# Kernel tuning notes

Hardware: AMD Instinct MI355X
Metric: run time of the kernel (lower is better)

Reference implementation:

```python
import jax, jax.numpy as jnp
import numpy as np

B, S, E, H = 2, 2048, 1024, 16
D = E // H          # head_dim = 64
HK = H // 4         # heads per kernel group = 4
MASKED_BIAS = -10000.0


def _dwconv_causal(x, w, b):
    # x: [B, h, S, D], w: [D, k], b: [D]; causal depthwise conv along S
    k = w.shape[1]
    s = x.shape[2]
    xp = jnp.pad(x, ((0, 0), (0, 0), (k - 1, 0), (0, 0)))
    out = b
    for i in range(k):
        out = out + xp[:, :, i:i + s, :] * w[:, i]
    return out


def setup_inputs() -> dict:
    key = jax.random.key(0)
    ks = jax.random.split(key, 32)
    inp = {
        'hidden_states': jax.random.normal(ks[0], (B, S, E), jnp.float32),
        'c_attn_w': jax.random.normal(ks[1], (E, 3 * E), jnp.float32) * 0.02,
        'c_attn_b': jnp.zeros((3 * E,), jnp.float32),
        'c_proj_w': jax.random.normal(ks[2], (E, E), jnp.float32) * 0.02,
        'c_proj_b': jnp.zeros((E,), jnp.float32),
    }
    i = 3
    for pre in ('q', 'k', 'v'):
        for kern in (3, 5, 7):
            inp[f'{pre}w{kern}'] = jax.random.normal(ks[i], (D, kern), jnp.float32) * (1.0 / kern)
            inp[f'{pre}b{kern}'] = jnp.zeros((D,), jnp.float32)
            i += 1
    return inp


def _forward(hidden_states, c_attn_w, c_attn_b, c_proj_w, c_proj_b,
             qw3, qb3, qw5, qb5, qw7, qb7,
             kw3, kb3, kw5, kb5, kw7, kb7,
             vw3, vb3, vw5, vb5, vw7, vb7):
    qkv = hidden_states @ c_attn_w + c_attn_b            # [B,S,3E]
    q, k, v = jnp.split(qkv, 3, axis=-1)

    def split_heads(t):
        return t.reshape(B, S, H, D).transpose(0, 2, 1, 3)  # [B,H,S,D]

    q, k, v = split_heads(q), split_heads(k), split_heads(v)

    def tranception_mix(t, ws_bs):
        parts = [t[:, :HK]]
        for g, (w, b) in enumerate(ws_bs):
            parts.append(_dwconv_causal(t[:, (g + 1) * HK:(g + 2) * HK], w, b))
        return jnp.concatenate(parts, axis=1)

    q = tranception_mix(q, [(qw3, qb3), (qw5, qb5), (qw7, qb7)])
    k = tranception_mix(k, [(kw3, kb3), (kw5, kb5), (kw7, kb7)])
    v = tranception_mix(v, [(vw3, vb3), (vw5, vb5), (vw7, vb7)])

    scores = jnp.einsum('bhqd,bhkd->bhqk', q, k) / jnp.sqrt(jnp.float32(D))
    causal = jnp.tril(jnp.ones((S, S), bool))
    scores = jnp.where(causal, scores, jnp.float32(MASKED_BIAS))
    attn = jax.nn.softmax(scores, axis=-1)
    out = jnp.einsum('bhqk,bhkd->bhqd', attn, v)
    out = out.transpose(0, 2, 1, 3).reshape(B, S, E)
    return out @ c_proj_w + c_proj_b


def reference(hidden_states, c_attn_w, c_attn_b, c_proj_w, c_proj_b,
              qw3, qb3, qw5, qb5, qw7, qb7,
              kw3, kb3, kw5, kb5, kw7, kb7,
              vw3, vb3, vw5, vb5, vw7, vb7):
    return _forward(hidden_states, c_attn_w, c_attn_b, c_proj_w, c_proj_b,
                    qw3, qb3, qw5, qb5, qw7, qb7,
                    kw3, kb3, kw5, kb5, kw7, kb7,
                    vw3, vb3, vw5, vb5, vw7, vb7)
```

## Files before the change

kernel.cpp:

```cpp
#include <hip/hip_runtime.h>
#include <stdint.h>
#include <math.h>

typedef unsigned short u16;
typedef __attribute__((ext_vector_type(8))) short short8;
typedef __attribute__((ext_vector_type(4))) float floatx4;

#define DEV static __device__ __forceinline__

struct alignas(8) us4 { u16 x, y, z, w; };
struct alignas(16) us8 { u16 v[8]; };
struct alignas(16) f4 { float x, y, z, w; };
struct alignas(8) f2 { float x, y; };
struct alignas(8) u32x2 { uint32_t x, y; };

DEV u16 f2bf(float f) {
  uint32_t u = __float_as_uint(f);
  u += 0x7fffu + ((u >> 16) & 1u);
  return (u16)(u >> 16);
}
DEV float bf2f(u16 h) { return __uint_as_float(((uint32_t)h) << 16); }

DEV uint32_t pkbf(float a, float b) {
#if __has_builtin(__builtin_amdgcn_cvt_pk_bf16_f32)
  typedef __attribute__((ext_vector_type(2))) __bf16 bf2_t;
  bf2_t v = __builtin_amdgcn_cvt_pk_bf16_f32(a, b);
  uint32_t r; __builtin_memcpy(&r, &v, 4); return r;
#else
  return (uint32_t)f2bf(a) | ((uint32_t)f2bf(b) << 16);
#endif
}

DEV float fexp2(float x) {
#if __has_builtin(__builtin_amdgcn_exp2f)
  return __builtin_amdgcn_exp2f(x);
#else
  return exp2f(x);
#endif
}

DEV void load_lds16(const void* g, void* l) {
  __builtin_amdgcn_global_load_lds((const __attribute__((address_space(1))) void*)g,
                                   (__attribute__((address_space(3))) void*)l, 16, 0, 0);
}

__global__ __launch_bounds__(256) void prep_fused(const float* __restrict__ hidden, u16* __restrict__ h_bf,
                                                  const float* __restrict__ attn_w, u16* __restrict__ wqkvT,
                                                  const float* __restrict__ proj_w, u16* __restrict__ wprojT) {
  __shared__ float tile[32][33];
  const int bx = blockIdx.x;
  const int t = threadIdx.x;
  if (bx < 4096) {
    const int i = (bx * 256 + t) * 4;
    f4 v = *(const f4*)(hidden + i);
    us4 o; o.x = f2bf(v.x); o.y = f2bf(v.y); o.z = f2bf(v.z); o.w = f2bf(v.w);
    *(us4*)(h_bf + i) = o;
    return;
  }
  const float* in; u16* out; int K, N, n0, k0;
  if (bx < 7168) {
    const int bid = bx - 4096;
    in = attn_w; out = wqkvT; K = 1024; N = 3072;
    n0 = (bid % 96) * 32; k0 = (bid / 96) * 32;
  } else {
    const int bid = bx - 7168;
    in = proj_w; out = wprojT; K = 1024; N = 1024;
    n0 = (bid & 31) * 32; k0 = (bid >> 5) * 32;
  }
  const int tx = t & 31, ty = t >> 5;
  for (int i = ty; i < 32; i += 8)
    tile[i][tx] = in[(size_t)(k0 + i) * N + n0 + tx];
  __syncthreads();
  for (int i = ty; i < 32; i += 8)
    out[(size_t)(n0 + i) * K + k0 + tx] = f2bf(tile[tx][i]);
}

template <int EPI, int BN, int NGRP>
__global__ __launch_bounds__(256) void gemm_bt(const u16* __restrict__ A,
                                               const u16* __restrict__ Bt,
                                               const float* __restrict__ bias,
                                               void* __restrict__ outp,
                                               int M, int N, int K) {
  constexpr int NT = BN / 32;
  __shared__ u16 lA[128 * 64];
  __shared__ u16 lB[BN * 64];
  const int t = threadIdx.x;
  const int w = t >> 6, lane = t & 63;
  const int quad = lane >> 4, l15 = lane & 15;
  const int wm = w >> 1, wn = w & 1;
  const int wn_off = wn * (BN / 2);

  const int bid = blockIdx.x;
  const int gsz = 32 * NGRP;
  const int grp = bid / gsz;
  const int r = bid - grp * gsz;
  const int m0 = (r & 31) * 128;
  const int n0 = (grp * NGRP + (r >> 5)) * BN;

  floatx4 acc[4][NT] = {};

  const int srow = t >> 3;
  const int scol = (((t & 7) ^ (srow & 7)) << 3);
  const u16* gA = A + (size_t)(m0 + srow) * K + scol;
  const u16* gB = Bt + (size_t)(n0 + srow) * K + scol;
  u16* sA = lA + t * 8;
  u16* sB = lB + t * 8;
  const size_t rstep = (size_t)32 * K;

  for (int k0 = 0; k0 < K; k0 += 64) {
#pragma unroll
    for (int c = 0; c < 4; c++) load_lds16(gA + c * rstep, sA + c * 2048);
#pragma unroll
    for (int c = 0; c < BN / 32; c++) load_lds16(gB + c * rstep, sB + c * 2048);
    gA += 64; gB += 64;
    __syncthreads();
#pragma unroll
    for (int kc = 0; kc < 2; kc++) {
      short8 af[4], bfr[NT];
#pragma unroll
      for (int mt = 0; mt < 4; mt++)
        af[mt] = *(const short8*)&lA[(wm * 64 + mt * 16 + l15) * 64 + (((kc * 4 + quad) ^ (l15 & 7)) << 3)];
#pragma unroll
      for (int nt = 0; nt < NT; nt++)
        bfr[nt] = *(const short8*)&lB[(wn_off + nt * 16 + l15) * 64 + (((kc * 4 + quad) ^ (l15 & 7)) << 3)];
#pragma unroll
      for (int mt = 0; mt < 4; mt++)
#pragma unroll
        for (int nt = 0; nt < NT; nt++)
          acc[mt][nt] = __builtin_amdgcn_mfma_f32_16x16x32_bf16(bfr[nt], af[mt], acc[mt][nt], 0, 0, 0);
    }
    __syncthreads();
  }

  if (EPI == 0) {
    u16* outq = (u16*)outp;
#pragma unroll
    for (int nt = 0; nt < NT; nt++) {
      const int nb = n0 + wn_off + nt * 16 + quad * 4;
      const f4 bn4 = *(const f4*)&bias[nb];
      const int tensor = nb >> 10, e = nb & 1023;
      const int h = e >> 6, d = e & 63;
      const size_t abase = (size_t)tensor * 4194304 + (size_t)h * 131072 + d;
#pragma unroll
      for (int mt = 0; mt < 4; mt++) {
        const int rr = m0 + wm * 64 + mt * 16 + l15;
        const int b = rr >> 11, s = rr & 2047;
        u32x2 o;
        o.x = pkbf(acc[mt][nt][0] + bn4.x, acc[mt][nt][1] + bn4.y);
        o.y = pkbf(acc[mt][nt][2] + bn4.z, acc[mt][nt][3] + bn4.w);
        *(u32x2*)&outq[abase + (size_t)b * 2097152 + (size_t)s * 64] = o;
      }
    }
  } else {
    float* outf = (float*)outp;
#pragma unroll
    for (int nt = 0; nt < NT; nt++) {
      const int nb = n0 + wn_off + nt * 16 + quad * 4;
      const f4 bn4 = *(const f4*)&bias[nb];
#pragma unroll
      for (int mt = 0; mt < 4; mt++) {
        const int rr = m0 + wm * 64 + mt * 16 + l15;
        f4 o;
        o.x = acc[mt][nt][0] + bn4.x;
        o.y = acc[mt][nt][1] + bn4.y;
        o.z = acc[mt][nt][2] + bn4.z;
        o.w = acc[mt][nt][3] + bn4.w;
        *(f4*)&outf[(size_t)rr * N + nb] = o;
      }
    }
  }
}

struct ConvW { const float* w[9]; const float* b[9]; };

template <int K>
DEV void conv_run(const u16* xt, int sl0, int d, const float* wp, const float* bp,
                  float qscale, float* out32) {
  float wr[K];
#pragma unroll
  for (int j = 0; j < K; j++) wr[j] = wp[d * K + j];
  const float br = bp[d];
  float win[K];
#pragma unroll
  for (int m = 1; m < K; m++) win[m] = bf2f(xt[(sl0 + 6 - K + m) * 68 + d]);
#pragma unroll
  for (int i = 0; i < 32; i++) {
#pragma unroll
    for (int m = 0; m < K - 1; m++) win[m] = win[m + 1];
    win[K - 1] = bf2f(xt[(sl0 + 6 + i) * 68 + d]);
    float val = br;
#pragma unroll
    for (int j = 0; j < K; j++) val += wr[j] * win[j];
    out32[i] = val * qscale;
  }
}

__global__ __launch_bounds__(256) void conv_mix(const u16* __restrict__ qkv, ConvW cw,
                                                u16* __restrict__ qpost,
                                                u16* __restrict__ kpost,
                                                u16* __restrict__ vpostT) {
  __shared__ u16 xt[134 * 68];
  __shared__ u16 yt[64 * 136];
  const int t = threadIdx.x;
  const int s0 = blockIdx.x * 128;
  const int h = blockIdx.y;
  const int tz = blockIdx.z;
  const int tensor = tz >> 1, b = tz & 1;
  const u16* src = qkv + (((size_t)tensor * 2 + b) * 16 + h) * 131072;

  for (int idx = t; idx < 134 * 16; idx += 256) {
    const int row = idx >> 4, c4 = (idx & 15) << 2;
    const int s = s0 - 6 + row;
    us4 v = {0, 0, 0, 0};
    if (s >= 0) v = *(const us4*)&src[(size_t)s * 64 + c4];
    *(us4*)&xt[row * 68 + c4] = v;
  }
  __syncthreads();

  const int group = h >> 2;
  const float* wp = (group > 0) ? cw.w[tensor * 3 + group - 1] : nullptr;
  const float* bp = (group > 0) ? cw.b[tensor * 3 + group - 1] : nullptr;
  const float qscale = (tensor == 0) ? 0.18033688f : 1.0f;

  const int d = t & 63;
  const int sl0 = (t >> 6) * 32;

  float out32[32];
  if (group == 0) {
#pragma unroll
    for (int i = 0; i < 32; i++)
      out32[i] = bf2f(xt[(sl0 + 6 + i) * 68 + d]) * qscale;
  } else if (group == 1) {
    conv_run<3>(xt, sl0, d, wp, bp, qscale, out32);
  } else if (group == 2) {
    conv_run<5>(xt, sl0, d, wp, bp, qscale, out32);
  } else {
    conv_run<7>(xt, sl0, d, wp, bp, qscale, out32);
  }

  if (tensor < 2) {
    u16* outp = (tensor == 0) ? qpost : kpost;
    const size_t ob = (((size_t)b * 16 + h) * 2048 + s0) * 64;
#pragma unroll
    for (int i = 0; i < 32; i++)
      outp[ob + (size_t)(sl0 + i) * 64 + d] = f2bf(out32[i]);
  } else {
#pragma unroll
    for (int i = 0; i < 32; i++)
      yt[d * 136 + sl0 + i] = f2bf(out32[i]);
    __syncthreads();
    const size_t ob = ((size_t)b * 16 + h) * 64;
    const int sl = (t & 15) * 8;
#pragma unroll
    for (int pass = 0; pass < 4; pass++) {
      const int dd = (t >> 4) + pass * 16;
      us8 vv = *(const us8*)&yt[dd * 136 + sl];
      *(us8*)&vpostT[(ob + dd) * 2048 + s0 + sl] = vv;
    }
  }
}

__global__ __launch_bounds__(256) void attn_fwd(const u16* __restrict__ Q,
                                                const u16* __restrict__ Kp,
                                                const u16* __restrict__ Vt,
                                                u16* __restrict__ Out,
                                                u16* __restrict__ Opart,
                                                f2* __restrict__ ml) {
  __shared__ u16 lK[2][128 * 64];
  __shared__ u16 lV[2][64 * 128];
  __shared__ u16 lP[4][32 * 64];
  const int t = threadIdx.x;
  const int w = t >> 6, lane = t & 63;
  const int quad = lane >> 4, l15 = lane & 15;
  const int e7 = l15 & 7;

  const int lin = blockIdx.x;
  const int xcd = lin & 7;
  const int idx = lin >> 3;
  const int grp = idx / 72;
  const int u = idx - grp * 72;
  const int bh = grp * 8 + xcd;
  int p = (int)(0.5f * (sqrtf(4.0f * (float)u + 1.0f) - 1.0f));
  if ((p + 1) * (p + 2) <= u) p++;
  if (p * (p + 1) > u) p--;
  const int v = u - p * (p + 1);
  const int qi = 2 * p + (v >= p + 1 ? 1 : 0);
  const int slab = v - (v >= p + 1 ? p + 1 : 0);
  const int ns = (qi + 2) >> 1;
  const int jbeg = slab * 2;
  const int nh = min(2, qi + 1 - jbeg);

  const int b = bh >> 4, h = bh & 15;
  const size_t qkbase = (size_t)bh * 131072;
  const int qblk = qi * 128 + w * 32;

  const int krow = t >> 3;
  const int kcol = (((t & 7) ^ (krow & 7)) << 3);
  const u16* gK = Kp + qkbase + (size_t)krow * 64 + kcol;
  const int vrow = t >> 4;
  const int vcol = (((t & 15) ^ vrow) << 3);
  const u16* gV = Vt + qkbase + (size_t)vrow * 2048 + vcol;
  u16* myP = lP[w];

  {
    const int j0 = jbeg * 128;
    u16* sK = &lK[0][0] + t * 8;
    u16* sV = &lV[0][0] + t * 8;
#pragma unroll
    for (int c = 0; c < 4; c++) {
      load_lds16(gK + (size_t)(j0 + c * 32) * 64, sK + c * 2048);
      load_lds16(gV + j0 + c * 16 * 2048, sV + c * 2048);
    }
  }
  asm volatile("" ::: "memory");

  short8 qf[2][2];
#pragma unroll
  for (int qt = 0; qt < 2; qt++)
#pragma unroll
    for (int kc = 0; kc < 2; kc++)
      qf[qt][kc] = *(const short8*)&Q[qkbase + (size_t)(qblk + qt * 16 + l15) * 64 + kc * 32 + quad * 8];
  asm volatile("" ::: "memory");

  if (nh == 2) {
    const int j0 = (jbeg + 1) * 128;
    u16* sK = &lK[1][0] + t * 8;
    u16* sV = &lV[1][0] + t * 8;
#pragma unroll
    for (int c = 0; c < 4; c++) {
      load_lds16(gK + (size_t)(j0 + c * 32) * 64, sK + c * 2048);
      load_lds16(gV + j0 + c * 16 * 2048, sV + c * 2048);
    }
    asm volatile("s_waitcnt vmcnt(12)" ::: "memory");
  } else {
    asm volatile("s_waitcnt vmcnt(4)" ::: "memory");
  }
  __builtin_amdgcn_s_barrier();

  float lst[2] = {0.0f, 0.0f};
  floatx4 accO[4][2] = {};

  for (int hf = 0; hf < nh; hf++) {
    if (hf == 1) {
      asm volatile("s_waitcnt vmcnt(0)" ::: "memory");
      __builtin_amdgcn_s_barrier();
    }
    const int j = jbeg + hf;
    const int j0 = j * 128;
    const u16* cK = lK[hf];
    const u16* cV = lV[hf];

    floatx4 accS[8][2] = {};
    __builtin_amdgcn_s_setprio(1);
#pragma unroll
    for (int kvt = 0; kvt < 8; kvt++) {
#pragma unroll
      for (int kc = 0; kc < 2; kc++) {
        const short8 a = *(const short8*)&cK[(kvt * 16 + l15) * 64 + (((kc * 4 + quad) ^ e7) << 3)];
#pragma unroll
        for (int qt = 0; qt < 2; qt++)
          accS[kvt][qt] = __builtin_amdgcn_mfma_f32_16x16x32_bf16(a, qf[qt][kc], accS[kvt][qt], 0, 0, 0);
      }
    }
    __builtin_amdgcn_s_setprio(0);

    if (j == qi) {
#pragma unroll
      for (int qt = 0; qt < 2; qt++) {
        const int q = qblk + qt * 16 + l15;
#pragma unroll
        for (int kvt = 0; kvt < 8; kvt++)
#pragma unroll
          for (int r = 0; r < 4; r++) {
            const int kv = j0 + kvt * 16 + quad * 4 + r;
            if (kv > q) accS[kvt][qt][r] = -3.0e38f;
          }
      }
    }

    uint32_t pk01[2][8], pk23[2][8];
#pragma unroll
    for (int qt = 0; qt < 2; qt++) {
      float ts = 0.0f;
#pragma unroll
      for (int kvt = 0; kvt < 8; kvt++) {
        const float p0 = fexp2(accS[kvt][qt][0]);
        const float p1 = fexp2(accS[kvt][qt][1]);
        const float p2 = fexp2(accS[kvt][qt][2]);
        const float p3 = fexp2(accS[kvt][qt][3]);
        ts += (p0 + p1) + (p2 + p3);
        pk01[qt][kvt] = pkbf(p0, p1);
        pk23[qt][kvt] = pkbf(p2, p3);
      }
      lst[qt] += ts;
    }

#pragma unroll
    for (int kvh = 0; kvh < 2; kvh++) {
#pragma unroll
      for (int qt = 0; qt < 2; qt++) {
        const int prow = (qt * 16 + l15) * 64;
#pragma unroll
        for (int kt = 0; kt < 4; kt++) {
          const int kvt = kvh * 4 + kt;
          const int slot = (kt * 2 + (quad >> 1)) ^ e7;
          u32x2 pk; pk.x = pk01[qt][kvt]; pk.y = pk23[qt][kvt];
          *(u32x2*)&myP[prow + slot * 8 + (quad & 1) * 4] = pk;
        }
      }
      asm volatile("s_waitcnt lgkmcnt(0)" ::: "memory");
      __builtin_amdgcn_s_setprio(1);
#pragma unroll
      for (int kk = 0; kk < 2; kk++) {
        const int kvc = kvh * 2 + kk;
        short8 pf[2];
#pragma unroll
        for (int qt = 0; qt < 2; qt++)
          pf[qt] = *(const short8*)&myP[(qt * 16 + l15) * 64 + (((kk * 4 + quad) ^ e7) << 3)];
#pragma unroll
        for (int dt = 0; dt < 4; dt++) {
          const short8 vf = *(const short8*)&cV[(dt * 16 + l15) * 128 + (((kvc * 4 + quad) ^ l15) << 3)];
#pragma unroll
          for (int qt = 0; qt < 2; qt++)
            accO[dt][qt] = __builtin_amdgcn_mfma_f32_16x16x32_bf16(vf, pf[qt], accO[dt][qt], 0, 0, 0);
        }
      }
      __builtin_amdgcn_s_setprio(0);
    }
  }

#pragma unroll
  for (int qt = 0; qt < 2; qt++) {
    lst[qt] += __shfl_xor(lst[qt], 16);
    lst[qt] += __shfl_xor(lst[qt], 32);
  }

  if (ns == 1) {
#pragma unroll
    for (int qt = 0; qt < 2; qt++) {
      const float inv = 1.0f / lst[qt];
      const int q = qblk + qt * 16 + l15;
#pragma unroll
      for (int dt = 0; dt < 4; dt++) {
        u32x2 o;
        o.x = pkbf(accO[dt][qt][0] * inv, accO[dt][qt][1] * inv);
        o.y = pkbf(accO[dt][qt][2] * inv, accO[dt][qt][3] * inv);
        *(u32x2*)&Out[((size_t)b * 2048 + q) * 1024 + h * 64 + dt * 16 + quad * 4] = o;
      }
    }
  } else {
    const int slot = bh * 72 + u;
    u16* op = Opart + (size_t)slot * 8192;
#pragma unroll
    for (int qt = 0; qt < 2; qt++) {
      const int ql = w * 32 + qt * 16 + l15;
#pragma unroll
      for (int dt = 0; dt < 4; dt++) {
        u32x2 o;
        o.x = pkbf(accO[dt][qt][0], accO[dt][qt][1]);
        o.y = pkbf(accO[dt][qt][2], accO[dt][qt][3]);
        *(u32x2*)&op[(size_t)ql * 64 + dt * 16 + quad * 4] = o;
      }
      if (quad == 0) {
        f2 v2; v2.x = 0.0f; v2.y = lst[qt];
        ml[slot * 128 + ql] = v2;
      }
    }
  }
}

__global__ __launch_bounds__(256) void attn_reduce(const u16* __restrict__ Opart,
                                                   const f2* __restrict__ ml,
                                                   u16* __restrict__ Out) {
  const int qi = blockIdx.x + 2;
  const int bh = blockIdx.y;
  const int b = bh >> 4, h = bh & 15;
  const int p = qi >> 1;
  const int base = bh * 72 + p * (p + 1) + (qi & 1) * (p + 1);
  const int ns = (qi + 2) >> 1;
  const int t = threadIdx.x;
  const int q = t >> 1, dh = (t & 1) * 32;

  float m[8], l[8], wgt[8];
  float mmax = -3.0e38f;
  for (int s = 0; s < ns; s++) {
    f2 v = ml[(base + s) * 128 + q];
    m[s] = v.x; l[s] = v.y;
    mmax = fmaxf(mmax, m[s]);
  }
  float lsum = 0.0f;
  for (int s = 0; s < ns; s++) {
    wgt[s] = fexp2(m[s] - mmax);
    lsum += wgt[s] * l[s];
  }
  float acc[32] = {};
  for (int s = 0; s < ns; s++) {
    const u16* src = Opart + ((size_t)(base + s) * 128 + q) * 64 + dh;
    const float ws = wgt[s];
#pragma unroll
    for (int i = 0; i < 8; i++) {
      us4 vv = *(const us4*)&src[i * 4];
      acc[i * 4 + 0] += ws * bf2f(vv.x);
      acc[i * 4 + 1] += ws * bf2f(vv.y);
      acc[i * 4 + 2] += ws * bf2f(vv.z);
      acc[i * 4 + 3] += ws * bf2f(vv.w);
    }
  }
  const float inv = 1.0f / lsum;
  u16* dst = Out + ((size_t)b * 2048 + qi * 128 + q) * 1024 + h * 64 + dh;
#pragma unroll
  for (int i = 0; i < 8; i++) {
    u32x2 o;
    o.x = pkbf(acc[i * 4 + 0] * inv, acc[i * 4 + 1] * inv);
    o.y = pkbf(acc[i * 4 + 2] * inv, acc[i * 4 + 3] * inv);
    *(u32x2*)&dst[i * 4] = o;
  }
}

extern "C" void kernel_launch(void* const* d_in, const int* in_sizes, int n_in,
                              void* d_out, int out_size, void* d_ws, size_t ws_size,
                              hipStream_t stream) {
  (void)in_sizes; (void)n_in; (void)out_size; (void)ws_size;
  const float* hidden = (const float*)d_in[0];
  const float* attn_w = (const float*)d_in[1];
  const float* attn_b = (const float*)d_in[2];
  const float* proj_w = (const float*)d_in[3];
  const float* proj_b = (const float*)d_in[4];
  ConvW cw;
  for (int i = 0; i < 9; i++) {
    cw.w[i] = (const float*)d_in[5 + 2 * i];
    cw.b[i] = (const float*)d_in[6 + 2 * i];
  }

  uint8_t* ws = (uint8_t*)d_ws;
  u16* h_bf   = (u16*)(ws + 0);
  u16* wqkvT  = (u16*)(ws + 8388608);
  u16* qkvpre = (u16*)(ws + 14680064);
  u16* qpost  = (u16*)(ws + 39845888);
  u16* kpost  = (u16*)(ws + 48234496);
  u16* vpostT = (u16*)(ws + 56623104);
  u16* attno  = (u16*)(ws + 65011712);
  u16* wprojT = (u16*)(ws + 73400320);
  f2*  ml     = (f2*) (ws + 75497472);
  u16* Opart  = (u16*)(ws + 0);

  prep_fused<<<8192, 256, 0, stream>>>(hidden, h_bf, attn_w, wqkvT, proj_w, wprojT);
  gemm_bt<0, 128, 6><<<768, 256, 0, stream>>>(h_bf, wqkvT, attn_b, (void*)qkvpre, 4096, 3072, 1024);
  conv_mix<<<dim3(16, 16, 6), 256, 0, stream>>>(qkvpre, cw, qpost, kpost, vpostT);
  attn_fwd<<<dim3(2304), 256, 0, stream>>>(qpost, kpost, vpostT, attno, Opart, ml);
  attn_reduce<<<dim3(14, 32), 256, 0, stream>>>(Opart, ml, attno);
  gemm_bt<1, 64, 8><<<512, 256, 0, stream>>>(attno, wprojT, proj_b, d_out, 4096, 1024, 1024);
}
```

Measured before the change: 250.9 us.

## Single-buffer K/V tiles and shrink P staging to raise attention occupancy

The attention kernel drops its double-buffered K/V LDS tiles in favour of a single buffer that is loaded synchronously at the start of each half. It also halves the per-wave P staging area by writing P in 32-wide kv chunks with a new XOR swizzle. Launch bounds now request 4 blocks per CU. LDS use falls from 80KB to about 40KB per block so more blocks can be resident, at the cost of losing the prefetch overlap of the second K/V tile and adding a barrier plus a full vmcnt wait per half.

```diff
diff --git a/kernel.cpp b/kernel.cpp
--- a/kernel.cpp
+++ b/kernel.cpp
@@ -260,19 +260,20 @@
   }
 }
 
-__global__ __launch_bounds__(256) void attn_fwd(const u16* __restrict__ Q,
-                                                const u16* __restrict__ Kp,
-                                                const u16* __restrict__ Vt,
-                                                u16* __restrict__ Out,
-                                                u16* __restrict__ Opart,
-                                                f2* __restrict__ ml) {
-  __shared__ u16 lK[2][128 * 64];
-  __shared__ u16 lV[2][64 * 128];
-  __shared__ u16 lP[4][32 * 64];
+__global__ __launch_bounds__(256, 4) void attn_fwd(const u16* __restrict__ Q,
+                                                   const u16* __restrict__ Kp,
+                                                   const u16* __restrict__ Vt,
+                                                   u16* __restrict__ Out,
+                                                   u16* __restrict__ Opart,
+                                                   f2* __restrict__ ml) {
+  __shared__ u16 lK[128 * 64];
+  __shared__ u16 lV[64 * 128];
+  __shared__ u16 lP[4][32 * 32];
   const int t = threadIdx.x;
   const int w = t >> 6, lane = t & 63;
   const int quad = lane >> 4, l15 = lane & 15;
   const int e7 = l15 & 7;
+  const int px = (l15 >> 1) & 3;
 
   const int lin = blockIdx.x;
   const int xcd = lin & 7;
@@ -302,53 +303,32 @@
   const u16* gV = Vt + qkbase + (size_t)vrow * 2048 + vcol;
   u16* myP = lP[w];
 
-  {
-    const int j0 = jbeg * 128;
-    u16* sK = &lK[0][0] + t * 8;
-    u16* sV = &lV[0][0] + t * 8;
-#pragma unroll
-    for (int c = 0; c < 4; c++) {
-      load_lds16(gK + (size_t)(j0 + c * 32) * 64, sK + c * 2048);
-      load_lds16(gV + j0 + c * 16 * 2048, sV + c * 2048);
-    }
-  }
-  asm volatile("" ::: "memory");
-
   short8 qf[2][2];
 #pragma unroll
   for (int qt = 0; qt < 2; qt++)
 #pragma unroll
     for (int kc = 0; kc < 2; kc++)
       qf[qt][kc] = *(const short8*)&Q[qkbase + (size_t)(qblk + qt * 16 + l15) * 64 + kc * 32 + quad * 8];
-  asm volatile("" ::: "memory");
-
-  if (nh == 2) {
-    const int j0 = (jbeg + 1) * 128;
-    u16* sK = &lK[1][0] + t * 8;
-    u16* sV = &lV[1][0] + t * 8;
-#pragma unroll
-    for (int c = 0; c < 4; c++) {
-      load_lds16(gK + (size_t)(j0 + c * 32) * 64, sK + c * 2048);
-      load_lds16(gV + j0 + c * 16 * 2048, sV + c * 2048);
-    }
-    asm volatile("s_waitcnt vmcnt(12)" ::: "memory");
-  } else {
-    asm volatile("s_waitcnt vmcnt(4)" ::: "memory");
-  }
-  __builtin_amdgcn_s_barrier();
 
   float lst[2] = {0.0f, 0.0f};
   floatx4 accO[4][2] = {};
 
   for (int hf = 0; hf < nh; hf++) {
-    if (hf == 1) {
-      asm volatile("s_waitcnt vmcnt(0)" ::: "memory");
-      __builtin_amdgcn_s_barrier();
-    }
     const int j = jbeg + hf;
     const int j0 = j * 128;
-    const u16* cK = lK[hf];
-    const u16* cV = lV[hf];
+
+    if (hf) __builtin_amdgcn_s_barrier();
+    {
+      u16* sK = lK + t * 8;
+      u16* sV = lV + t * 8;
+#pragma unroll
+      for (int c = 0; c < 4; c++) {
+        load_lds16(gK + (size_t)(j0 + c * 32) * 64, sK + c * 2048);
+        load_lds16(gV + j0 + c * 16 * 2048, sV + c * 2048);
+      }
+    }
+    asm volatile("s_waitcnt vmcnt(0)" ::: "memory");
+    __builtin_amdgcn_s_barrier();
 
     floatx4 accS[8][2] = {};
     __builtin_amdgcn_s_setprio(1);
@@ -356,7 +336,7 @@
     for (int kvt = 0; kvt < 8; kvt++) {
 #pragma unroll
       for (int kc = 0; kc < 2; kc++) {
-        const short8 a = *(const short8*)&cK[(kvt * 16 + l15) * 64 + (((kc * 4 + quad) ^ e7) << 3)];
+        const short8 a = *(const short8*)&lK[(kvt * 16 + l15) * 64 + (((kc * 4 + quad) ^ e7) << 3)];
 #pragma unroll
         for (int qt = 0; qt < 2; qt++)
           accS[kvt][qt] = __builtin_amdgcn_mfma_f32_16x16x32_bf16(a, qf[qt][kc], accS[kvt][qt], 0, 0, 0);
@@ -396,34 +376,30 @@
     }
 
 #pragma unroll
-    for (int kvh = 0; kvh < 2; kvh++) {
+    for (int kvq = 0; kvq < 4; kvq++) {
 #pragma unroll
       for (int qt = 0; qt < 2; qt++) {
-        const int prow = (qt * 16 + l15) * 64;
-#pragma unroll
-        for (int kt = 0; kt < 4; kt++) {
-          const int kvt = kvh * 4 + kt;
-          const int slot = (kt * 2 + (quad >> 1)) ^ e7;
+        const int prow = (qt * 16 + l15) * 32;
+#pragma unroll
+        for (int kt = 0; kt < 2; kt++) {
+          const int kvt = kvq * 2 + kt;
+          const int bb = (kt * 2 + (quad >> 1)) ^ px;
           u32x2 pk; pk.x = pk01[qt][kvt]; pk.y = pk23[qt][kvt];
-          *(u32x2*)&myP[prow + slot * 8 + (quad & 1) * 4] = pk;
+          *(u32x2*)&myP[prow + bb * 8 + (quad & 1) * 4] = pk;
         }
       }
       asm volatile("s_waitcnt lgkmcnt(0)" ::: "memory");
       __builtin_amdgcn_s_setprio(1);
-#pragma unroll
-      for (int kk = 0; kk < 2; kk++) {
-        const int kvc = kvh * 2 + kk;
-        short8 pf[2];
+      short8 pf[2];
+#pragma unroll
+      for (int qt = 0; qt < 2; qt++)
+        pf[qt] = *(const short8*)&myP[(qt * 16 + l15) * 32 + ((quad ^ px) << 3)];
+#pragma unroll
+      for (int dt = 0; dt < 4; dt++) {
+        const short8 vf = *(const short8*)&lV[(dt * 16 + l15) * 128 + (((kvq * 4 + quad) ^ l15) << 3)];
 #pragma unroll
         for (int qt = 0; qt < 2; qt++)
-          pf[qt] = *(const short8*)&myP[(qt * 16 + l15) * 64 + (((kk * 4 + quad) ^ e7) << 3)];
-#pragma unroll
-        for (int dt = 0; dt < 4; dt++) {
-          const short8 vf = *(const short8*)&cV[(dt * 16 + l15) * 128 + (((kvc * 4 + quad) ^ l15) << 3)];
-#pragma unroll
-          for (int qt = 0; qt < 2; qt++)
-            accO[dt][qt] = __builtin_amdgcn_mfma_f32_16x16x32_bf16(vf, pf[qt], accO[dt][qt], 0, 0, 0);
-        }
+          accO[dt][qt] = __builtin_amdgcn_mfma_f32_16x16x32_bf16(vf, pf[qt], accO[dt][qt], 0, 0, 0);
       }
       __builtin_amdgcn_s_setprio(0);
     }
```

Result: slower. 289.1 us (+15.2%).

## Replace split-KV attention with one block per query tile and drop reduce kernel

Applied to the files above, without the earlier changes.

Attention no longer splits each query tile's key range into two-block slabs with a separate reduction kernel. Each block now walks every causal key block for one 128-row query tile, double-buffering K/V tiles in LDS, and writes normalized output directly. Query tiles are paired light and heavy across the grid order to balance load. This removes the partial-output writes, the reduce launch and its memory traffic, but cuts the grid from 2304 to 512 blocks. That lowers parallelism and leaves a long serial loop for the last query tiles.

```diff
diff --git a/kernel.cpp b/kernel.cpp
--- a/kernel.cpp
+++ b/kernel.cpp
@@ -263,9 +263,7 @@
 __global__ __launch_bounds__(256) void attn_fwd(const u16* __restrict__ Q,
                                                 const u16* __restrict__ Kp,
                                                 const u16* __restrict__ Vt,
-                                                u16* __restrict__ Out,
-                                                u16* __restrict__ Opart,
-                                                f2* __restrict__ ml) {
+                                                u16* __restrict__ Out) {
   __shared__ u16 lK[2][128 * 64];
   __shared__ u16 lV[2][64 * 128];
   __shared__ u16 lP[4][32 * 64];
@@ -276,19 +274,11 @@
 
   const int lin = blockIdx.x;
   const int xcd = lin & 7;
-  const int idx = lin >> 3;
-  const int grp = idx / 72;
-  const int u = idx - grp * 72;
+  const int s = lin >> 3;
+  const int grp = s & 3;
+  const int qsel = s >> 2;
   const int bh = grp * 8 + xcd;
-  int p = (int)(0.5f * (sqrtf(4.0f * (float)u + 1.0f) - 1.0f));
-  if ((p + 1) * (p + 2) <= u) p++;
-  if (p * (p + 1) > u) p--;
-  const int v = u - p * (p + 1);
-  const int qi = 2 * p + (v >= p + 1 ? 1 : 0);
-  const int slab = v - (v >= p + 1 ? p + 1 : 0);
-  const int ns = (qi + 2) >> 1;
-  const int jbeg = slab * 2;
-  const int nh = min(2, qi + 1 - jbeg);
+  const int qi = (qsel < 8) ? qsel : 23 - qsel;
 
   const int b = bh >> 4, h = bh & 15;
   const size_t qkbase = (size_t)bh * 131072;
@@ -302,53 +292,45 @@
   const u16* gV = Vt + qkbase + (size_t)vrow * 2048 + vcol;
   u16* myP = lP[w];
 
+  short8 qf[2][2];
+#pragma unroll
+  for (int qt = 0; qt < 2; qt++)
+#pragma unroll
+    for (int kc = 0; kc < 2; kc++)
+      qf[qt][kc] = *(const short8*)&Q[qkbase + (size_t)(qblk + qt * 16 + l15) * 64 + kc * 32 + quad * 8];
+
   {
-    const int j0 = jbeg * 128;
     u16* sK = &lK[0][0] + t * 8;
     u16* sV = &lV[0][0] + t * 8;
 #pragma unroll
     for (int c = 0; c < 4; c++) {
-      load_lds16(gK + (size_t)(j0 + c * 32) * 64, sK + c * 2048);
-      load_lds16(gV + j0 + c * 16 * 2048, sV + c * 2048);
-    }
-  }
-  asm volatile("" ::: "memory");
-
-  short8 qf[2][2];
-#pragma unroll
-  for (int qt = 0; qt < 2; qt++)
-#pragma unroll
-    for (int kc = 0; kc < 2; kc++)
-      qf[qt][kc] = *(const short8*)&Q[qkbase + (size_t)(qblk + qt * 16 + l15) * 64 + kc * 32 + quad * 8];
-  asm volatile("" ::: "memory");
-
-  if (nh == 2) {
-    const int j0 = (jbeg + 1) * 128;
-    u16* sK = &lK[1][0] + t * 8;
-    u16* sV = &lV[1][0] + t * 8;
-#pragma unroll
-    for (int c = 0; c < 4; c++) {
-      load_lds16(gK + (size_t)(j0 + c * 32) * 64, sK + c * 2048);
-      load_lds16(gV + j0 + c * 16 * 2048, sV + c * 2048);
-    }
-    asm volatile("s_waitcnt vmcnt(12)" ::: "memory");
-  } else {
-    asm volatile("s_waitcnt vmcnt(4)" ::: "memory");
-  }
+      load_lds16(gK + (size_t)(c * 32) * 64, sK + c * 2048);
+      load_lds16(gV + c * 16 * 2048, sV + c * 2048);
+    }
+  }
+  asm volatile("s_waitcnt vmcnt(0)" ::: "memory");
   __builtin_amdgcn_s_barrier();
 
   float lst[2] = {0.0f, 0.0f};
   floatx4 accO[4][2] = {};
 
-  for (int hf = 0; hf < nh; hf++) {
-    if (hf == 1) {
-      asm volatile("s_waitcnt vmcnt(0)" ::: "memory");
-      __builtin_amdgcn_s_barrier();
-    }
-    const int j = jbeg + hf;
+  for (int j = 0; j <= qi; ++j) {
+    const int cur = j & 1;
+
+    if (j < qi) {
+      const int j0n = (j + 1) * 128;
+      u16* sK = &lK[cur ^ 1][0] + t * 8;
+      u16* sV = &lV[cur ^ 1][0] + t * 8;
+#pragma unroll
+      for (int c = 0; c < 4; c++) {
+        load_lds16(gK + (size_t)(j0n + c * 32) * 64, sK + c * 2048);
+        load_lds16(gV + j0n + c * 16 * 2048, sV + c * 2048);
+      }
+    }
+
     const int j0 = j * 128;
-    const u16* cK = lK[hf];
-    const u16* cV = lV[hf];
+    const u16* cK = lK[cur];
+    const u16* cV = lV[cur];
 
     floatx4 accS[8][2] = {};
     __builtin_amdgcn_s_setprio(1);
@@ -427,6 +409,11 @@
       }
       __builtin_amdgcn_s_setprio(0);
     }
+
+    if (j < qi) {
+      asm volatile("s_waitcnt vmcnt(0)" ::: "memory");
+      __builtin_amdgcn_s_barrier();
+    }
   }
 
 #pragma unroll
@@ -435,85 +422,17 @@
     lst[qt] += __shfl_xor(lst[qt], 32);
   }
 
-  if (ns == 1) {
-#pragma unroll
-    for (int qt = 0; qt < 2; qt++) {
-      const float inv = 1.0f / lst[qt];
-      const int q = qblk + qt * 16 + l15;
-#pragma unroll
-      for (int dt = 0; dt < 4; dt++) {
-        u32x2 o;
-        o.x = pkbf(accO[dt][qt][0] * inv, accO[dt][qt][1] * inv);
-        o.y = pkbf(accO[dt][qt][2] * inv, accO[dt][qt][3] * inv);
-        *(u32x2*)&Out[((size_t)b * 2048 + q) * 1024 + h * 64 + dt * 16 + quad * 4] = o;
-      }
-    }
-  } else {
-    const int slot = bh * 72 + u;
-    u16* op = Opart + (size_t)slot * 8192;
-#pragma unroll
-    for (int qt = 0; qt < 2; qt++) {
-      const int ql = w * 32 + qt * 16 + l15;
-#pragma unroll
-      for (int dt = 0; dt < 4; dt++) {
-        u32x2 o;
-        o.x = pkbf(accO[dt][qt][0], accO[dt][qt][1]);
-        o.y = pkbf(accO[dt][qt][2], accO[dt][qt][3]);
-        *(u32x2*)&op[(size_t)ql * 64 + dt * 16 + quad * 4] = o;
-      }
-      if (quad == 0) {
-        f2 v2; v2.x = 0.0f; v2.y = lst[qt];
-        ml[slot * 128 + ql] = v2;
-      }
-    }
-  }
-}
-
-__global__ __launch_bounds__(256) void attn_reduce(const u16* __restrict__ Opart,
-                                                   const f2* __restrict__ ml,
-                                                   u16* __restrict__ Out) {
-  const int qi = blockIdx.x + 2;
-  const int bh = blockIdx.y;
-  const int b = bh >> 4, h = bh & 15;
-  const int p = qi >> 1;
-  const int base = bh * 72 + p * (p + 1) + (qi & 1) * (p + 1);
-  const int ns = (qi + 2) >> 1;
-  const int t = threadIdx.x;
-  const int q = t >> 1, dh = (t & 1) * 32;
-
-  float m[8], l[8], wgt[8];
-  float mmax = -3.0e38f;
-  for (int s = 0; s < ns; s++) {
-    f2 v = ml[(base + s) * 128 + q];
-    m[s] = v.x; l[s] = v.y;
-    mmax = fmaxf(mmax, m[s]);
-  }
-  float lsum = 0.0f;
-  for (int s = 0; s < ns; s++) {
-    wgt[s] = fexp2(m[s] - mmax);
-    lsum += wgt[s] * l[s];
-  }
-  float acc[32] = {};
-  for (int s = 0; s < ns; s++) {
-    const u16* src = Opart + ((size_t)(base + s) * 128 + q) * 64 + dh;
-    const float ws = wgt[s];
-#pragma unroll
-    for (int i = 0; i < 8; i++) {
-      us4 vv = *(const us4*)&src[i * 4];
-      acc[i * 4 + 0] += ws * bf2f(vv.x);
-      acc[i * 4 + 1] += ws * bf2f(vv.y);
-      acc[i * 4 + 2] += ws * bf2f(vv.z);
-      acc[i * 4 + 3] += ws * bf2f(vv.w);
-    }
-  }
-  const float inv = 1.0f / lsum;
-  u16* dst = Out + ((size_t)b * 2048 + qi * 128 + q) * 1024 + h * 64 + dh;
-#pragma unroll
-  for (int i = 0; i < 8; i++) {
-    u32x2 o;
-    o.x = pkbf(acc[i * 4 + 0] * inv, acc[i * 4 + 1] * inv);
-    o.y = pkbf(acc[i * 4 + 2] * inv, acc[i * 4 + 3] * inv);
-    *(u32x2*)&dst[i * 4] = o;
+#pragma unroll
+  for (int qt = 0; qt < 2; qt++) {
+    const float inv = 1.0f / lst[qt];
+    const int q = qblk + qt * 16 + l15;
+#pragma unroll
+    for (int dt = 0; dt < 4; dt++) {
+      u32x2 o;
+      o.x = pkbf(accO[dt][qt][0] * inv, accO[dt][qt][1] * inv);
+      o.y = pkbf(accO[dt][qt][2] * inv, accO[dt][qt][3] * inv);
+      *(u32x2*)&Out[((size_t)b * 2048 + q) * 1024 + h * 64 + dt * 16 + quad * 4] = o;
+    }
   }
 }
 
@@ -541,13 +460,10 @@
   u16* vpostT = (u16*)(ws + 56623104);
   u16* attno  = (u16*)(ws + 65011712);
   u16* wprojT = (u16*)(ws + 73400320);
-  f2*  ml     = (f2*) (ws + 75497472);
-  u16* Opart  = (u16*)(ws + 0);
 
   prep_fused<<<8192, 256, 0, stream>>>(hidden, h_bf, attn_w, wqkvT, proj_w, wprojT);
   gemm_bt<0, 128, 6><<<768, 256, 0, stream>>>(h_bf, wqkvT, attn_b, (void*)qkvpre, 4096, 3072, 1024);
   conv_mix<<<dim3(16, 16, 6), 256, 0, stream>>>(qkvpre, cw, qpost, kpost, vpostT);
-  attn_fwd<<<dim3(2304), 256, 0, stream>>>(qpost, kpost, vpostT, attno, Opart, ml);
-  attn_reduce<<<dim3(14, 32), 256, 0, stream>>>(Opart, ml, attno);
+  attn_fwd<<<dim3(512), 256, 0, stream>>>(qpost, kpost, vpostT, attno);
   gemm_bt<1, 64, 8><<<512, 256, 0, stream>>>(attno, wprojT, proj_b, d_out, 4096, 1024, 1024);
 }
```

Result: faster. 240.5 us (-4.1%).
